# Kernel optimization log

Measured on AMD Instinct MI355X. Metric: run time of the kernel, lower is better.

The kernel has to match this reference:

```python
import jax, jax.numpy as jnp
from jax import lax
import numpy as np

B, C, H, W = 4, 1024, 64, 64
HEAD_DIM = 8
HEADS = C // HEAD_DIM  # 128
EPS = 1e-15
BN_EPS = 1e-5
DN = ('NCHW', 'OIHW', 'NCHW')


def setup_inputs() -> dict:
    key = jax.random.key(0)
    ks = jax.random.split(key, 8)
    s = lambda k, shp, scale: jax.random.normal(k, shp, jnp.float32) * scale
    return {
        'x': s(ks[0], (B, C, H, W), 1.0),
        'Wq': s(ks[1], (C, C), C ** -0.5),
        'Wk': s(ks[2], (C, C), C ** -0.5),
        'Wv': s(ks[3], (C, C), C ** -0.5),
        'dw_w': s(ks[4], (3 * C, 1, 5, 5), 0.2),          # depthwise, groups=3C
        'pw_w': s(ks[5], (3 * C, HEAD_DIM, 1, 1), 0.3),   # 1x1 grouped, groups=3*heads
        'Wout': s(ks[6], (C, 2 * C), (2 * C) ** -0.5),
        'gamma': jnp.ones((C,), jnp.float32),
        'beta': jnp.zeros((C,), jnp.float32),
    }


def _forward(x, Wq, Wk, Wv, dw_w, pw_w, Wout, gamma, beta):
    b, c, h, w = x.shape
    n = h * w
    hbhwc = jnp.moveaxis(x, 1, -1)                      # B H W C
    q = hbhwc @ Wq.T
    k = hbhwc @ Wk.T
    v = hbhwc @ Wv.T
    qkv = jnp.moveaxis(jnp.concatenate([q, k, v], -1), -1, 1)  # B 3C H W
    # multiscale branch: depthwise kxk then grouped 1x1
    ms = lax.conv_general_dilated(qkv, dw_w, (1, 1), 'SAME',
                                  feature_group_count=3 * c, dimension_numbers=DN)
    ms = lax.conv_general_dilated(ms, pw_w, (1, 1), 'VALID',
                                  feature_group_count=3 * HEADS, dimension_numbers=DN)
    hs = jnp.concatenate([qkv, ms], axis=1)             # B 6C H W
    hs = hs.astype(jnp.float32).reshape(b, -1, 3 * HEAD_DIM, n)  # B ht 3d N
    q, k, v = jnp.split(hs, 3, axis=2)                  # each B ht d N
    q = jax.nn.relu(q)
    k = jax.nn.relu(k)
    v = jnp.pad(v, ((0, 0), (0, 0), (0, 1), (0, 0)), constant_values=1.0)  # B ht d+1 N
    scores = jnp.einsum('bhdn,bhen->bhde', v, k)        # B ht d+1 d
    out = jnp.einsum('bhde,bhen->bhdn', scores, q)      # B ht d+1 N
    out = out[:, :, :-1] / (out[:, :, -1:] + EPS)       # B ht d N
    out = out.reshape(b, -1, h, w)                      # B 2C H W
    out = jnp.moveaxis(jnp.moveaxis(out, 1, -1) @ Wout.T, -1, 1)  # B C H W
    # batch norm (batch statistics, affine)
    mean = out.mean(axis=(0, 2, 3), keepdims=True)
    var = out.var(axis=(0, 2, 3), keepdims=True)
    gb = lambda p: p[None, :, None, None]
    return (out - mean) * lax.rsqrt(var + BN_EPS) * gb(gamma) + gb(beta)


def reference(x, Wq, Wk, Wv, dw_w, pw_w, Wout, gamma, beta):
    return _forward(x, Wq, Wk, Wv, dw_w, pw_w, Wout, gamma, beta)
```

## Files before the change

kernel.cpp:

```cpp
#include <hip/hip_runtime.h>


typedef short bf16x8 __attribute__((ext_vector_type(8)));
typedef float f32x4 __attribute__((ext_vector_type(4)));

__device__ __forceinline__ float bf2f(unsigned short u) {
  union { unsigned int i; float f; } w; w.i = ((unsigned int)u) << 16; return w.f;
}
__device__ __forceinline__ unsigned short f2bf(float f) {
  union { float f; unsigned int i; } w; w.f = f;
  return (unsigned short)((w.i + 0x7fffu + ((w.i >> 16) & 1u)) >> 16);
}

__device__ __forceinline__ void gload16(const void* g, void* l) {
  __builtin_amdgcn_global_load_lds(
      (const __attribute__((address_space(1))) void*)g,
      (__attribute__((address_space(3))) void*)l, 16, 0, 0);
}

static constexpr int BB = 4, CC = 1024, NN = 4096;
static constexpr int C3 = 3 * CC;
static constexpr int C2 = 2 * CC;
static constexpr int MROWS = BB * NN;

__global__ __launch_bounds__(256) void k_transpose_both(const float* __restrict__ x,
                                                        float* __restrict__ xTf,
                                                        unsigned short* __restrict__ xTb) {
  __shared__ float tile[32][33];
  const int c0 = blockIdx.y << 5, n0 = blockIdx.x << 5;
  const int tx = threadIdx.x & 31, ty = threadIdx.x >> 5;
#pragma unroll
  for (int i = 0; i < 32; i += 8)
    tile[ty + i][tx] = x[((size_t)(c0 + ty + i)) * NN + n0 + tx];
  __syncthreads();
#pragma unroll
  for (int i = 0; i < 32; i += 8) {
    const float v = tile[tx][ty + i];
    const size_t idx = ((size_t)(n0 + ty + i)) * CC + c0 + tx;
    xTf[idx] = v;
    xTb[idx] = f2bf(v);
  }
}

__global__ void k_cvt(const float* __restrict__ src, unsigned short* __restrict__ dst, int n4) {
  int i = blockIdx.x * 256 + threadIdx.x;
  if (i < n4) {
    float4 v = ((const float4*)src)[i];
    ushort4 o;
    o.x = f2bf(v.x); o.y = f2bf(v.y); o.z = f2bf(v.z); o.w = f2bf(v.w);
    ((ushort4*)dst)[i] = o;
  }
}

__global__ __launch_bounds__(256) void k_wpack(const float* __restrict__ Wq,
                                               const float* __restrict__ Wk,
                                               const float* __restrict__ Wv,
                                               float* __restrict__ Wpack) {
  const int j = blockIdx.x;
  const int c = 24 * (j >> 3) + (j & 7);
  const float* src = (c < CC) ? (Wq + (size_t)c * CC)
                   : (c < 2 * CC) ? (Wk + (size_t)(c - CC) * CC)
                   : (Wv + (size_t)(c - 2 * CC) * CC);
  const int t = threadIdx.x;
  ((float4*)(Wpack + (size_t)j * CC))[t] = ((const float4*)src)[t];
}

__global__ __launch_bounds__(256) void k_wkv(const float* __restrict__ Wq,
                                             const float* __restrict__ Wk,
                                             const float* __restrict__ Wv,
                                             unsigned short* __restrict__ Wkv) {
  const int jj = blockIdx.x;
  const int c = 24 * (jj >> 4) + 8 + (jj & 15);
  const float* src = (c < CC) ? (Wq + (size_t)c * CC)
                   : (c < 2 * CC) ? (Wk + (size_t)(c - CC) * CC)
                   : (Wv + (size_t)(c - 2 * CC) * CC);
  const int t = threadIdx.x;
  float4 v = ((const float4*)src)[t];
  ushort4 o;
  o.x = f2bf(v.x); o.y = f2bf(v.y); o.z = f2bf(v.z); o.w = f2bf(v.w);
  ((ushort4*)(Wkv + (size_t)jj * CC))[t] = o;
}

__global__ __launch_bounds__(256) void gemm_kv(const unsigned short* __restrict__ A,
                                               const unsigned short* __restrict__ Bmat,
                                               float* __restrict__ qkvT) {
  __shared__ __align__(16) unsigned short lA[128 * 32];
  __shared__ __align__(16) unsigned short lB[128 * 32];
  const int bx = blockIdx.x, by = blockIdx.y;
  const int tid = threadIdx.x, lane = tid & 63, wid = tid >> 6;
  const int wm = wid >> 1, wn = wid & 1;
  const int K = CC;

  const int srow = wid * 32 + (lane >> 2);
  const int skoff = (lane & 3) * 8;
  const unsigned short* Ag = A + (size_t)(bx * 128 + srow) * K + skoff;
  const unsigned short* Bg = Bmat + (size_t)(by * 128 + srow) * K + skoff;
  unsigned short* lAw = &lA[(wid * 32) * 32];
  unsigned short* lBw = &lB[(wid * 32) * 32];

  f32x4 acc[4][4] = {};

  for (int kt = 0; kt < K; kt += 32) {
    gload16(Ag + kt, lAw);
    gload16(Ag + kt + (size_t)16 * K, lAw + 16 * 32);
    gload16(Bg + kt, lBw);
    gload16(Bg + kt + (size_t)16 * K, lBw + 16 * 32);
    __syncthreads();

    const int fr = lane & 15, fkk = (lane >> 4) * 8;
    bf16x8 af[4], bfr[4];
#pragma unroll
    for (int i = 0; i < 4; ++i) {
      af[i]  = *reinterpret_cast<const bf16x8*>(&lA[(wm * 64 + i * 16 + fr) * 32 + fkk]);
      bfr[i] = *reinterpret_cast<const bf16x8*>(&lB[(wn * 64 + i * 16 + fr) * 32 + fkk]);
    }
#pragma unroll
    for (int i = 0; i < 4; ++i)
#pragma unroll
      for (int j = 0; j < 4; ++j)
        acc[i][j] = __builtin_amdgcn_mfma_f32_16x16x32_bf16(af[i], bfr[j], acc[i][j], 0, 0, 0);
    __syncthreads();
  }

  const int fr = lane & 15, fg = lane >> 4;
#pragma unroll
  for (int i = 0; i < 4; ++i) {
    const int row0 = bx * 128 + wm * 64 + i * 16 + fg * 4;
#pragma unroll
    for (int j = 0; j < 4; ++j) {
      const int jj = by * 128 + wn * 64 + j * 16 + fr;
      const int c = 24 * (jj >> 4) + 8 + (jj & 15);
#pragma unroll
      for (int r = 0; r < 4; ++r)
        qkvT[(size_t)(row0 + r) * C3 + c] = acc[i][j][r];
    }
  }
}

__global__ __launch_bounds__(256) void gemm_bt(const unsigned short* __restrict__ A,
                                               const unsigned short* __restrict__ Bmat,
                                               float* __restrict__ Cout,
                                               int M, int N, int K) {
  __shared__ __align__(16) unsigned short lA[128 * 32];
  __shared__ __align__(16) unsigned short lB[128 * 32];
  const int bx = blockIdx.x, by = blockIdx.y;
  const int tid = threadIdx.x, lane = tid & 63, wid = tid >> 6;
  const int wm = wid >> 1, wn = wid & 1;

  const int srow = wid * 32 + (lane >> 2);
  const int skoff = (lane & 3) * 8;
  const unsigned short* Ag = A + (size_t)(bx * 128 + srow) * K + skoff;
  const unsigned short* Bg = Bmat + (size_t)(by * 128 + srow) * K + skoff;
  unsigned short* lAw = &lA[(wid * 32) * 32];
  unsigned short* lBw = &lB[(wid * 32) * 32];

  f32x4 acc[4][4] = {};

  for (int kt = 0; kt < K; kt += 32) {
    gload16(Ag + kt, lAw);
    gload16(Ag + kt + (size_t)16 * K, lAw + 16 * 32);
    gload16(Bg + kt, lBw);
    gload16(Bg + kt + (size_t)16 * K, lBw + 16 * 32);
    __syncthreads();

    const int fr = lane & 15, fkk = (lane >> 4) * 8;
    bf16x8 af[4], bfr[4];
#pragma unroll
    for (int i = 0; i < 4; ++i) {
      af[i]  = *reinterpret_cast<const bf16x8*>(&lA[(wm * 64 + i * 16 + fr) * 32 + fkk]);
      bfr[i] = *reinterpret_cast<const bf16x8*>(&lB[(wn * 64 + i * 16 + fr) * 32 + fkk]);
    }
#pragma unroll
    for (int i = 0; i < 4; ++i)
#pragma unroll
      for (int j = 0; j < 4; ++j)
        acc[i][j] = __builtin_amdgcn_mfma_f32_16x16x32_bf16(af[i], bfr[j], acc[i][j], 0, 0, 0);
    __syncthreads();
  }

  const int fr = lane & 15, fg = lane >> 4;
#pragma unroll
  for (int i = 0; i < 4; ++i) {
    const int row0 = bx * 128 + wm * 64 + i * 16 + fg * 4;
#pragma unroll
    for (int j = 0; j < 4; ++j) {
      const int col = by * 128 + wn * 64 + j * 16 + fr;
#pragma unroll
      for (int r = 0; r < 4; ++r)
        Cout[(size_t)(row0 + r) * N + col] = acc[i][j][r];
    }
  }
}

__global__ __launch_bounds__(512) void k_qnp(const float* __restrict__ xTf,
                                             const float* __restrict__ Wpack,
                                             float* __restrict__ qkvT) {
  __shared__ float lA[16][132];
  __shared__ float lB[16][132];
  const int bm = blockIdx.x * 128, bj = blockIdx.y * 128;
  const int t = threadIdx.x;
  const int mat = t >> 8;
  const int rr = (t & 255) >> 1;
  const int hh = t & 1;
  const float* gsrc = mat ? (Wpack + (size_t)(bj + rr) * CC + hh * 8)
                          : (xTf  + (size_t)(bm + rr) * CC + hh * 8);
  const int tj = t & 15, tm = t >> 4;

  float acc[2][4][4] = {};

  for (int k0 = 0; k0 < CC; k0 += 16) {
    const float4 g0 = *(const float4*)(gsrc + k0);
    const float4 g1 = *(const float4*)(gsrc + k0 + 4);
    __syncthreads();
    float (*dst)[132] = mat ? lB : lA;
    dst[hh * 8 + 0][rr] = g0.x; dst[hh * 8 + 1][rr] = g0.y;
    dst[hh * 8 + 2][rr] = g0.z; dst[hh * 8 + 3][rr] = g0.w;
    dst[hh * 8 + 4][rr] = g1.x; dst[hh * 8 + 5][rr] = g1.y;
    dst[hh * 8 + 6][rr] = g1.z; dst[hh * 8 + 7][rr] = g1.w;
    __syncthreads();
#pragma unroll
    for (int kk = 0; kk < 16; ++kk) {
      const float4 av  = *(const float4*)&lA[kk][tm * 4];
      const float4 bv0 = *(const float4*)&lB[kk][tj * 4];
      const float4 bv1 = *(const float4*)&lB[kk][64 + tj * 4];
      const float af[4]  = {av.x, av.y, av.z, av.w};
      const float bf0[4] = {bv0.x, bv0.y, bv0.z, bv0.w};
      const float bf1[4] = {bv1.x, bv1.y, bv1.z, bv1.w};
#pragma unroll
      for (int i = 0; i < 4; ++i)
#pragma unroll
        for (int j = 0; j < 4; ++j) {
          acc[0][i][j] = fmaf(af[i], bf0[j], acc[0][i][j]);
          acc[1][i][j] = fmaf(af[i], bf1[j], acc[1][i][j]);
        }
    }
  }

#pragma unroll
  for (int i = 0; i < 4; ++i) {
    const int row = bm + tm * 4 + i;
#pragma unroll
    for (int jb = 0; jb < 2; ++jb)
#pragma unroll
      for (int j = 0; j < 4; ++j) {
        const int jj = bj + jb * 64 + tj * 4 + j;
        const int c = 24 * (jj >> 3) + (jj & 7);
        qkvT[(size_t)row * C3 + c] = acc[jb][i][j];
      }
  }
}

__global__ __launch_bounds__(256) void k_conv_ms(const float* __restrict__ qkvT,
                                                 const float* __restrict__ dw_w,
                                                 const float* __restrict__ pw_w,
                                                 float* __restrict__ msT) {
  __shared__ __align__(16) float tin[20][20][8];
  __shared__ float wdw[8][25];
  __shared__ float wpw[8][8];
  const int g = blockIdx.y;
  const int ty0 = (blockIdx.x >> 2) << 4, tx0 = (blockIdx.x & 3) << 4;
  const int tid = threadIdx.x;

  if (tid < 200) wdw[tid / 25][tid % 25] = dw_w[(size_t)(g * 8 + tid / 25) * 25 + tid % 25];
  if (tid < 64) wpw[tid >> 3][tid & 7] = pw_w[(size_t)(g * 8 + (tid >> 3)) * 8 + (tid & 7)];

  for (int p = tid; p < 400; p += 256) {
    const int iy = p / 20, ix = p % 20;
    const int gy = ty0 + iy - 2, gx = tx0 + ix - 2;
    float4 a = make_float4(0, 0, 0, 0), b4 = a;
    if (gy >= 0 && gy < 64 && gx >= 0 && gx < 64) {
      const float* s = &qkvT[((size_t)(gy * 64 + gx)) * C3 + g * 8];
      a = *(const float4*)s;
      b4 = *(const float4*)(s + 4);
    }
    *(float4*)&tin[iy][ix][0] = a;
    *(float4*)&tin[iy][ix][4] = b4;
  }
  __syncthreads();

  const int ty = tid >> 4, tx = tid & 15;
  double acc[8] = {0, 0, 0, 0, 0, 0, 0, 0};
#pragma unroll
  for (int dy = 0; dy < 5; ++dy)
#pragma unroll
    for (int dx = 0; dx < 5; ++dx) {
#pragma unroll
      for (int ci = 0; ci < 8; ++ci)
        acc[ci] += (double)wdw[ci][dy * 5 + dx] * (double)tin[ty + dy][tx + dx][ci];
    }
  float o[8];
#pragma unroll
  for (int co = 0; co < 8; ++co) {
    double s = 0.0;
#pragma unroll
    for (int ci = 0; ci < 8; ++ci) s += (double)wpw[co][ci] * acc[ci];
    o[co] = (float)s;
  }
  const int n = (ty0 + ty) * 64 + tx0 + tx;
  float* d = &msT[((size_t)n) * C3 + g * 8];
  *(float4*)d = make_float4(o[0], o[1], o[2], o[3]);
  *(float4*)(d + 4) = make_float4(o[4], o[5], o[6], o[7]);
}

__global__ __launch_bounds__(256) void k_attn(const float* __restrict__ qkvT,
                                              const float* __restrict__ msT,
                                              unsigned short* __restrict__ attn) {
  const int h = blockIdx.x;
  const float* src = (h < 128) ? qkvT + h * 24 : msT + (h - 128) * 24;
  const int tid = threadIdx.x, lane = tid & 63, wid = tid >> 6;

  float s[72];
#pragma unroll
  for (int i = 0; i < 72; ++i) s[i] = 0.f;

  for (int n = tid; n < NN; n += 256) {
    const float* p = src + (size_t)n * C3;
    float4 k0 = *(const float4*)(p + 8), k1 = *(const float4*)(p + 12);
    float4 v0 = *(const float4*)(p + 16), v1 = *(const float4*)(p + 20);
    float kf[8] = {fmaxf(k0.x, 0.f), fmaxf(k0.y, 0.f), fmaxf(k0.z, 0.f), fmaxf(k0.w, 0.f),
                   fmaxf(k1.x, 0.f), fmaxf(k1.y, 0.f), fmaxf(k1.z, 0.f), fmaxf(k1.w, 0.f)};
    float vf[8] = {v0.x, v0.y, v0.z, v0.w, v1.x, v1.y, v1.z, v1.w};
#pragma unroll
    for (int d = 0; d < 8; ++d)
#pragma unroll
      for (int e = 0; e < 8; ++e) s[d * 8 + e] += vf[d] * kf[e];
#pragma unroll
    for (int e = 0; e < 8; ++e) s[64 + e] += kf[e];
  }

  __shared__ float red[4][72];
  __shared__ float sc[72];
#pragma unroll
  for (int i = 0; i < 72; ++i) {
    float v = s[i];
#pragma unroll
    for (int off = 32; off > 0; off >>= 1) v += __shfl_xor(v, off, 64);
    if (lane == 0) red[wid][i] = v;
  }
  __syncthreads();
  if (tid < 72) sc[tid] = red[0][tid] + red[1][tid] + red[2][tid] + red[3][tid];
  __syncthreads();

  float sl[72];
#pragma unroll
  for (int i = 0; i < 72; ++i) sl[i] = sc[i];

  for (int n = tid; n < NN; n += 256) {
    const float* p = src + (size_t)n * C3;
    float4 q0 = *(const float4*)p, q1 = *(const float4*)(p + 4);
    float qf[8] = {fmaxf(q0.x, 0.f), fmaxf(q0.y, 0.f), fmaxf(q0.z, 0.f), fmaxf(q0.w, 0.f),
                   fmaxf(q1.x, 0.f), fmaxf(q1.y, 0.f), fmaxf(q1.z, 0.f), fmaxf(q1.w, 0.f)};
    float o[9];
#pragma unroll
    for (int d = 0; d < 9; ++d) {
      float t = 0.f;
#pragma unroll
      for (int e = 0; e < 8; ++e) t += sl[d * 8 + e] * qf[e];
      o[d] = t;
    }
    const float inv = 1.f / (o[8] + 1e-15f);
    union { unsigned short u[8]; uint4 v; } res;
#pragma unroll
    for (int d = 0; d < 8; ++d) res.u[d] = f2bf(o[d] * inv);
    *(uint4*)&attn[((size_t)n) * C2 + h * 8] = res.v;
  }
}

__global__ __launch_bounds__(256) void k_bn_stats(const float* __restrict__ out2,
                                                  float* __restrict__ part) {
  const int ch = blockIdx.x * 256 + threadIdx.x;
  const int r0 = blockIdx.y << 8;
  float s = 0.f, s2 = 0.f;
  for (int i = 0; i < 256; ++i) {
    float v = out2[(size_t)(r0 + i) * CC + ch];
    s += v; s2 += v * v;
  }
  part[((size_t)blockIdx.y * 2 + 0) * CC + ch] = s;
  part[((size_t)blockIdx.y * 2 + 1) * CC + ch] = s2;
}

__global__ __launch_bounds__(256) void k_bn_reduce(const float* __restrict__ part,
                                                   float* __restrict__ stats) {
  const int ch = blockIdx.x * 256 + threadIdx.x;
  float s = 0.f, s2 = 0.f;
  for (int i = 0; i < 64; ++i) {
    s += part[((size_t)i * 2 + 0) * CC + ch];
    s2 += part[((size_t)i * 2 + 1) * CC + ch];
  }
  stats[ch] = s;
  stats[CC + ch] = s2;
}

__global__ __launch_bounds__(256) void k_bn_apply(const float* __restrict__ out2,
                                                  const float* __restrict__ stats,
                                                  const float* __restrict__ gamma,
                                                  const float* __restrict__ beta,
                                                  float* __restrict__ out) {
  __shared__ float tile[32][33];
  const int b = blockIdx.z;
  const int c0 = blockIdx.y << 5, n0 = blockIdx.x << 5;
  const int tx = threadIdx.x & 31, ty = threadIdx.x >> 5;
  const int c = c0 + tx;
  const float mean = stats[c] * (1.f / 16384.f);
  const float var = stats[CC + c] * (1.f / 16384.f) - mean * mean;
  const float scale = gamma[c] * rsqrtf(var + 1e-5f);
  const float shift = beta[c] - mean * scale;
#pragma unroll
  for (int i = 0; i < 32; i += 8)
    tile[ty + i][tx] = out2[((size_t)b * NN + n0 + ty + i) * CC + c] * scale + shift;
  __syncthreads();
#pragma unroll
  for (int i = 0; i < 32; i += 8)
    out[((size_t)b * CC + c0 + ty + i) * NN + n0 + tx] = tile[tx][ty + i];
}

extern "C" void kernel_launch(void* const* d_in, const int* in_sizes, int n_in,
                              void* d_out, int out_size, void* d_ws, size_t ws_size,
                              hipStream_t stream) {
  const float* x     = (const float*)d_in[0];
  const float* Wq    = (const float*)d_in[1];
  const float* Wk    = (const float*)d_in[2];
  const float* Wv    = (const float*)d_in[3];
  const float* dw_w  = (const float*)d_in[4];
  const float* pw_w  = (const float*)d_in[5];
  const float* Wout  = (const float*)d_in[6];
  const float* gamma = (const float*)d_in[7];
  const float* beta  = (const float*)d_in[8];
  float* out = (float*)d_out;
  (void)ws_size; (void)in_sizes; (void)n_in; (void)out_size;

  char* ws = (char*)d_ws;
  const size_t MB = 1024 * 1024;
  float*          qkvT = (float*)(ws + 0);
  float*          msT  = (float*)(ws + 48 * MB);
  float*          xTf  = (float*)(ws + 96 * MB);
  unsigned short* xTb  = (unsigned short*)(ws + 112 * MB);
  unsigned short* Wkv  = (unsigned short*)(ws + 120 * MB);
  float*          Wpack= (float*)(ws + 126 * MB);
  unsigned short* WoutB= (unsigned short*)(ws + 130 * MB);
  float*          part = (float*)(ws + 134 * MB);
  float*          stats= (float*)(ws + 135 * MB);
  float*          out2 = (float*)(ws + 0);
  unsigned short* attnB= (unsigned short*)d_out;

  k_wkv<<<dim3(C2), 256, 0, stream>>>(Wq, Wk, Wv, Wkv);
  k_wpack<<<dim3(CC), 256, 0, stream>>>(Wq, Wk, Wv, Wpack);
  k_cvt<<<dim3(CC * C2 / 4 / 256), 256, 0, stream>>>(Wout, WoutB, CC * C2 / 4);

  for (int b = 0; b < BB; ++b) {
    k_transpose_both<<<dim3(NN / 32, CC / 32), 256, 0, stream>>>(x + (size_t)b * CC * NN, xTf, xTb);
    gemm_kv<<<dim3(NN / 128, C2 / 128), 256, 0, stream>>>(xTb, Wkv, qkvT);
    k_qnp<<<dim3(NN / 128, CC / 128), 512, 0, stream>>>(xTf, Wpack, qkvT);
    k_conv_ms<<<dim3(16, C3 / 8), 256, 0, stream>>>(qkvT, dw_w, pw_w, msT);
    k_attn<<<dim3(256), 256, 0, stream>>>(qkvT, msT, attnB + (size_t)b * NN * C2);
  }

  gemm_bt<<<dim3(MROWS / 128, CC / 128), 256, 0, stream>>>(attnB, WoutB, out2, MROWS, CC, C2);

  k_bn_stats<<<dim3(CC / 256, 64), 256, 0, stream>>>(out2, part);
  k_bn_reduce<<<dim3(CC / 256), 256, 0, stream>>>(part, stats);
  k_bn_apply<<<dim3(NN / 32, CC / 32, BB), 256, 0, stream>>>(out2, stats, gamma, beta, out);
}
```

Before: 1.385 ms.

## Rewrite fp32 Q projection GEMM with per-thread row and uniform weight loads

Replaces the 128x128 register-tiled fp32 SIMT GEMM for the Q projection with a kernel where each thread owns one output row and 32 output columns. Only the activation tile goes through LDS. Weights are read straight from global memory at wave-uniform addresses, which can become scalar loads. This removes the weight LDS staging and the transposed LDS stores. In exchange there is less register-level reuse of activations, many more global weight reads, and uncoalesced strided stores of 32 columns per row.

```diff
diff --git a/kernel.cpp b/kernel.cpp
--- a/kernel.cpp
+++ b/kernel.cpp
@@ -137,6 +137,63 @@
   }
 }
 
+__global__ __launch_bounds__(256) void k_qnp2(const float* __restrict__ xTf,
+                                              const float* __restrict__ Wpack,
+                                              float* __restrict__ qkvT) {
+  __shared__ float lA[256 * 20];
+  const int bm = blockIdx.x * 256;
+  const int bj = blockIdx.y * 32;
+  const int t = threadIdx.x;
+  const int m_loc = t;
+  const int srow = t >> 2, sq = t & 3;
+
+  float acc[32];
+#pragma unroll
+  for (int j = 0; j < 32; ++j) acc[j] = 0.f;
+
+  const float* wbase = Wpack + (size_t)bj * CC;
+
+  for (int kp = 0; kp < CC; kp += 16) {
+    float4 g[4];
+#pragma unroll
+    for (int r = 0; r < 4; ++r)
+      g[r] = *(const float4*)(xTf + (size_t)(bm + r * 64 + srow) * CC + kp + sq * 4);
+    __syncthreads();
+#pragma unroll
+    for (int r = 0; r < 4; ++r)
+      *(float4*)&lA[(r * 64 + srow) * 20 + sq * 4] = g[r];
+    __syncthreads();
+
+    const float* lam = &lA[m_loc * 20];
+    const float4 a0 = *(const float4*)(lam + 0);
+    const float4 a1 = *(const float4*)(lam + 4);
+    const float4 a2 = *(const float4*)(lam + 8);
+    const float4 a3 = *(const float4*)(lam + 12);
+#pragma unroll
+    for (int j = 0; j < 32; ++j) {
+      const float* wr = wbase + (size_t)j * CC + kp;
+      float s = acc[j];
+      s = fmaf(a0.x, wr[0], s);   s = fmaf(a0.y, wr[1], s);
+      s = fmaf(a0.z, wr[2], s);   s = fmaf(a0.w, wr[3], s);
+      s = fmaf(a1.x, wr[4], s);   s = fmaf(a1.y, wr[5], s);
+      s = fmaf(a1.z, wr[6], s);   s = fmaf(a1.w, wr[7], s);
+      s = fmaf(a2.x, wr[8], s);   s = fmaf(a2.y, wr[9], s);
+      s = fmaf(a2.z, wr[10], s);  s = fmaf(a2.w, wr[11], s);
+      s = fmaf(a3.x, wr[12], s);  s = fmaf(a3.y, wr[13], s);
+      s = fmaf(a3.z, wr[14], s);  s = fmaf(a3.w, wr[15], s);
+      acc[j] = s;
+    }
+  }
+
+  const int m = bm + m_loc;
+#pragma unroll
+  for (int j = 0; j < 32; ++j) {
+    const int jj = bj + j;
+    const int c = 24 * (jj >> 3) + (jj & 7);
+    qkvT[(size_t)m * C3 + c] = acc[j];
+  }
+}
+
 __global__ __launch_bounds__(256) void gemm_bt(const unsigned short* __restrict__ A,
                                                const unsigned short* __restrict__ Bmat,
                                                float* __restrict__ Cout,
@@ -189,64 +246,6 @@
       for (int r = 0; r < 4; ++r)
         Cout[(size_t)(row0 + r) * N + col] = acc[i][j][r];
     }
-  }
-}
-
-__global__ __launch_bounds__(512) void k_qnp(const float* __restrict__ xTf,
-                                             const float* __restrict__ Wpack,
-                                             float* __restrict__ qkvT) {
-  __shared__ float lA[16][132];
-  __shared__ float lB[16][132];
-  const int bm = blockIdx.x * 128, bj = blockIdx.y * 128;
-  const int t = threadIdx.x;
-  const int mat = t >> 8;
-  const int rr = (t & 255) >> 1;
-  const int hh = t & 1;
-  const float* gsrc = mat ? (Wpack + (size_t)(bj + rr) * CC + hh * 8)
-                          : (xTf  + (size_t)(bm + rr) * CC + hh * 8);
-  const int tj = t & 15, tm = t >> 4;
-
-  float acc[2][4][4] = {};
-
-  for (int k0 = 0; k0 < CC; k0 += 16) {
-    const float4 g0 = *(const float4*)(gsrc + k0);
-    const float4 g1 = *(const float4*)(gsrc + k0 + 4);
-    __syncthreads();
-    float (*dst)[132] = mat ? lB : lA;
-    dst[hh * 8 + 0][rr] = g0.x; dst[hh * 8 + 1][rr] = g0.y;
-    dst[hh * 8 + 2][rr] = g0.z; dst[hh * 8 + 3][rr] = g0.w;
-    dst[hh * 8 + 4][rr] = g1.x; dst[hh * 8 + 5][rr] = g1.y;
-    dst[hh * 8 + 6][rr] = g1.z; dst[hh * 8 + 7][rr] = g1.w;
-    __syncthreads();
-#pragma unroll
-    for (int kk = 0; kk < 16; ++kk) {
-      const float4 av  = *(const float4*)&lA[kk][tm * 4];
-      const float4 bv0 = *(const float4*)&lB[kk][tj * 4];
-      const float4 bv1 = *(const float4*)&lB[kk][64 + tj * 4];
-      const float af[4]  = {av.x, av.y, av.z, av.w};
-      const float bf0[4] = {bv0.x, bv0.y, bv0.z, bv0.w};
-      const float bf1[4] = {bv1.x, bv1.y, bv1.z, bv1.w};
-#pragma unroll
-      for (int i = 0; i < 4; ++i)
-#pragma unroll
-        for (int j = 0; j < 4; ++j) {
-          acc[0][i][j] = fmaf(af[i], bf0[j], acc[0][i][j]);
-          acc[1][i][j] = fmaf(af[i], bf1[j], acc[1][i][j]);
-        }
-    }
-  }
-
-#pragma unroll
-  for (int i = 0; i < 4; ++i) {
-    const int row = bm + tm * 4 + i;
-#pragma unroll
-    for (int jb = 0; jb < 2; ++jb)
-#pragma unroll
-      for (int j = 0; j < 4; ++j) {
-        const int jj = bj + jb * 64 + tj * 4 + j;
-        const int c = 24 * (jj >> 3) + (jj & 7);
-        qkvT[(size_t)row * C3 + c] = acc[jb][i][j];
-      }
   }
 }
 
@@ -450,7 +449,7 @@
   for (int b = 0; b < BB; ++b) {
     k_transpose_both<<<dim3(NN / 32, CC / 32), 256, 0, stream>>>(x + (size_t)b * CC * NN, xTf, xTb);
     gemm_kv<<<dim3(NN / 128, C2 / 128), 256, 0, stream>>>(xTb, Wkv, qkvT);
-    k_qnp<<<dim3(NN / 128, CC / 128), 512, 0, stream>>>(xTf, Wpack, qkvT);
+    k_qnp2<<<dim3(NN / 256, CC / 32), 256, 0, stream>>>(xTf, Wpack, qkvT);
     k_conv_ms<<<dim3(16, C3 / 8), 256, 0, stream>>>(qkvT, dw_w, pw_w, msT);
     k_attn<<<dim3(256), 256, 0, stream>>>(qkvT, msT, attnB + (size_t)b * NN * C2);
   }
```

Result: slower. 3.741 ms (+170.2%).
